# Kernel tuning notes

Measured on AMD Instinct MI355X. Metric: run time of the kernel, lower is better.

The kernel has to match this reference:

```python
import jax, jax.numpy as jnp
import numpy as np


def setup_inputs() -> dict:
    key = jax.random.key(0)
    k0, k1, k2, k3 = jax.random.split(key, 4)
    T, B, K, L, DEG = 2000, 2048, 64, 64, 3
    return {
        "currents": jax.random.normal(k0, (T, B), dtype=jnp.float32),
        "a": jax.random.normal(k1, (K,), dtype=jnp.float32) * 0.05,
        "b_lag": jax.random.normal(k2, (L,), dtype=jnp.float32) * 1e-3,
        "poly_coeff": jax.random.normal(k3, (1, DEG + 1), dtype=jnp.float32) * 0.3,
        "b_act": jnp.zeros((1,), dtype=jnp.float32),
        "max_current": jnp.full((1,), 100.0, dtype=jnp.float32),
        "max_firing_rate": jnp.full((1,), 100.0, dtype=jnp.float32),
    }


def _poly_act(z, poly_coeff, b_act, max_current, max_firing_rate):
    # PolynomialActivation.forward: x=(z-b)/max_current; poly=sum_d x^d * coeff_d^2
    x = (z - b_act[0]) / max_current[0]  # [B]
    deg = poly_coeff.shape[1] - 1
    coeff = (poly_coeff ** 2)[0]  # [deg+1]
    # build integer powers safely (negative bases) via repeated multiply
    pows = [jnp.ones_like(x)]
    for _ in range(deg):
        pows.append(pows[-1] * x)
    powers = jnp.stack(pows, axis=-1)  # [B, deg+1]
    poly = powers @ coeff  # [B]
    return jax.nn.relu(max_firing_rate[0] * jnp.tanh(poly))


def reference(currents, a, b_lag, poly_coeff, b_act, max_current, max_firing_rate):
    T, B = currents.shape
    K, L = a.shape[0], b_lag.shape[0]

    def step(carry, c_t):
        cur_buf, fs_buf = carry  # [B,K], [B,L]
        cur_buf = jnp.concatenate([cur_buf[:, 1:], c_t[:, None]], axis=1)
        x = cur_buf @ a                      # einsum('j,ij->i')
        y = 1000.0 * (fs_buf @ b_lag)        # einsum('j,ij->i')
        f = _poly_act(x + y, poly_coeff, b_act, max_current, max_firing_rate)
        fs_buf = jnp.concatenate([fs_buf[:, 1:], f[:, None]], axis=1)
        return (cur_buf, fs_buf), f

    init = (jnp.zeros((B, K), currents.dtype), jnp.zeros((B, L), currents.dtype))
    _, fs = jax.lax.scan(step, init, currents)  # fs: [T, B]
    return fs
```

## Files before the change

kernel.cpp:

```cpp
#include <hip/hip_runtime.h>

#define T_STEPS 2000
#define BATCH   2048

__global__ __launch_bounds__(256) void fused_kernel(
    const float* __restrict__ currents, const float* __restrict__ a,
    const float* __restrict__ b_lag, const float* __restrict__ poly_coeff,
    const float* __restrict__ b_act, const float* __restrict__ max_current,
    const float* __restrict__ max_firing_rate, float* __restrict__ out)
{
    int tid  = threadIdx.x;
    int lane = tid & 63;
    int wid  = tid >> 6;
    int b    = blockIdx.x * 4 + wid;

    float inv = 1.0f / max_current[0];
    float cba = -b_act[0] * inv;
    float af  = a[63 - lane] * inv;
    float gam = (1000.0f * inv) * b_lag[63 - lane];

    const float K2 = 2.8853900817779268f;
    float c0 = poly_coeff[0], c1 = poly_coeff[1], c2 = poly_coeff[2], c3 = poly_coeff[3];
    float k0 = K2 * c0 * c0, k1 = K2 * c1 * c1, k2 = K2 * c2 * c2, k3 = K2 * c3 * c3;
    float M  = max_firing_rate[0];
    float m2 = -2.0f * M;

    auto bcast = [](float v, int l) {
        return __builtin_bit_cast(float,
            __builtin_amdgcn_readlane(__builtin_bit_cast(int, v), l));
    };
    auto rotl1 = [](float v) {
        int i = __builtin_bit_cast(int, v);
        return __builtin_bit_cast(float,
            __builtin_amdgcn_update_dpp(i, i, 0x134, 0xf, 0xf, false));
    };

    const float* ccol   = currents + b;
    float*       outcol = out + b;

    float R  = cba;
    float cv = ccol[(long)lane * BATCH];
    float fv = 0.0f;

    auto step = [&](int s) {
        float c = bcast(cv, s);
        R = fmaf(af, c, R);
        float u = bcast(R, 0);
        float u2 = u * u;
        float a1 = fmaf(u, k1, k0);
        float a2 = fmaf(u, k3, k2);
        float p  = fmaf(u2, a2, a1);
        float e  = __builtin_amdgcn_exp2f(p);
        float r  = __builtin_amdgcn_rcpf(e + 1.0f);
        float f  = fmaxf(fmaf(m2, r, M), 0.0f);
        float Rr = rotl1(R);
        Rr = (lane == 63) ? cba : Rr;
        R  = fmaf(gam, f, Rr);
        fv = (lane == s) ? f : fv;
    };

    for (int chunk = 0; chunk < 31; ++chunk) {
        int t0 = chunk * 64;
        int tp = t0 + 64 + lane;
        float cv_next = (tp < T_STEPS) ? ccol[(long)tp * BATCH] : 0.0f;
#pragma unroll
        for (int s = 0; s < 64; ++s) step(s);
        outcol[(long)(t0 + lane) * BATCH] = fv;
        cv = cv_next;
    }
#pragma unroll
    for (int s = 0; s < 16; ++s) step(s);
    if (lane < 16) outcol[(long)(1984 + lane) * BATCH] = fv;
}

extern "C" void kernel_launch(void* const* d_in, const int* in_sizes, int n_in,
                              void* d_out, int out_size, void* d_ws, size_t ws_size,
                              hipStream_t stream) {
    const float* currents   = (const float*)d_in[0];
    const float* a          = (const float*)d_in[1];
    const float* b_lag      = (const float*)d_in[2];
    const float* poly_coeff = (const float*)d_in[3];
    const float* b_act      = (const float*)d_in[4];
    const float* mc         = (const float*)d_in[5];
    const float* mfr        = (const float*)d_in[6];
    float* out = (float*)d_out;

    fused_kernel<<<BATCH / 4, 256, 0, stream>>>(
        currents, a, b_lag, poly_coeff, b_act, mc, mfr, out);
}
```

Baseline: 211.3 us.

## Split into parallel convolution kernel and packed 16-column recurrence kernel

Moves the feed-forward FIR over currents out of the serial loop into a separate, fully parallel convolution kernel that writes pre-activations into the output buffer. The recurrence kernel then packs 16 batch columns per wave, four lanes per column each holding 16 lag taps in a register ring, and uses quad DPP broadcasts instead of readlane. The aim is to shorten the per-step serial dependency chain and use more lanes per wave. In exchange it adds an extra pass over memory, a large unrolled register footprint, and only 128 single-wave blocks for the recurrence.

New measurement: 253.6 us. 1.2x slower.

```diff
diff --git a/kernel.cpp b/kernel.cpp
--- a/kernel.cpp
+++ b/kernel.cpp
@@ -2,75 +2,132 @@
 
 #define T_STEPS 2000
 #define BATCH   2048
+#define TT      16
+#define NCHUNK  125
 
-__global__ __launch_bounds__(256) void fused_kernel(
+template<int CTRL>
+__device__ __forceinline__ float dppf(float v) {
+    int i = __builtin_bit_cast(int, v);
+    return __builtin_bit_cast(float,
+        __builtin_amdgcn_update_dpp(i, i, CTRL, 0xf, 0xf, true));
+}
+
+__global__ __launch_bounds__(64) void conv_kernel(
     const float* __restrict__ currents, const float* __restrict__ a,
-    const float* __restrict__ b_lag, const float* __restrict__ poly_coeff,
     const float* __restrict__ b_act, const float* __restrict__ max_current,
-    const float* __restrict__ max_firing_rate, float* __restrict__ out)
+    float* __restrict__ X)
 {
-    int tid  = threadIdx.x;
-    int lane = tid & 63;
-    int wid  = tid >> 6;
-    int b    = blockIdx.x * 4 + wid;
+    int lane = threadIdx.x;
+    int t0   = blockIdx.x * TT;
+    int c    = blockIdx.y * 64 + lane;
 
     float inv = 1.0f / max_current[0];
-    float cba = -b_act[0] * inv;
-    float af  = a[63 - lane] * inv;
-    float gam = (1000.0f * inv) * b_lag[63 - lane];
+    float cb  = -b_act[0] * inv;
+
+    float cur[TT + 63];
+#pragma unroll
+    for (int rr = 0; rr < TT + 63; ++rr) {
+        int r = t0 - 63 + rr;
+        cur[rr] = (r >= 0) ? currents[(long)r * BATCH + c] : 0.0f;
+    }
+#pragma unroll
+    for (int i = 0; i < TT; ++i) {
+        float acc = 0.0f;
+#pragma unroll
+        for (int k = 0; k < 64; ++k)
+            acc = fmaf(a[k], cur[i + k], acc);
+        X[(long)(t0 + i) * BATCH + c] = fmaf(acc, inv, cb);
+    }
+}
+
+__global__ __launch_bounds__(64) void rec_kernel(
+    const float* X,
+    const float* __restrict__ b_lag, const float* __restrict__ poly_coeff,
+    const float* __restrict__ max_current, const float* __restrict__ max_firing_rate,
+    float* out)
+{
+    int lane = threadIdx.x;
+    int q    = lane & 3;
+    int cc   = lane >> 2;
+    long col = (long)blockIdx.x * 16 + cc;
+
+    float inv    = 1.0f / max_current[0];
+    float gscale = 1000.0f * inv;
+    float tap[16];
+#pragma unroll
+    for (int j = 0; j < 16; ++j)
+        tap[j] = gscale * b_lag[63 - (16 * q + j)];
 
     const float K2 = 2.8853900817779268f;
     float c0 = poly_coeff[0], c1 = poly_coeff[1], c2 = poly_coeff[2], c3 = poly_coeff[3];
-    float k0 = K2 * c0 * c0, k1 = K2 * c1 * c1, k2 = K2 * c2 * c2, k3 = K2 * c3 * c3;
+    float k0 = K2*c0*c0, k1 = K2*c1*c1, k2 = K2*c2*c2, k3 = K2*c3*c3;
     float M  = max_firing_rate[0];
     float m2 = -2.0f * M;
 
-    auto bcast = [](float v, int l) {
-        return __builtin_bit_cast(float,
-            __builtin_amdgcn_readlane(__builtin_bit_cast(int, v), l));
-    };
-    auto rotl1 = [](float v) {
-        int i = __builtin_bit_cast(int, v);
-        return __builtin_bit_cast(float,
-            __builtin_amdgcn_update_dpp(i, i, 0x134, 0xf, 0xf, false));
-    };
+    bool e0 = (q == 0), e1 = (q == 1), e2 = (q == 2), q3 = (q == 3);
 
-    const float* ccol   = currents + b;
-    float*       outcol = out + b;
+    float ring[16];
+#pragma unroll
+    for (int j = 0; j < 16; ++j) ring[j] = 0.0f;
 
-    float R  = cba;
-    float cv = ccol[(long)lane * BATCH];
-    float fv = 0.0f;
+    const float* xp = X + col;
+    float*       op = out + col;
 
-    auto step = [&](int s) {
-        float c = bcast(cv, s);
-        R = fmaf(af, c, R);
-        float u = bcast(R, 0);
-        float u2 = u * u;
-        float a1 = fmaf(u, k1, k0);
-        float a2 = fmaf(u, k3, k2);
-        float p  = fmaf(u2, a2, a1);
-        float e  = __builtin_amdgcn_exp2f(p);
-        float r  = __builtin_amdgcn_rcpf(e + 1.0f);
-        float f  = fmaxf(fmaf(m2, r, M), 0.0f);
-        float Rr = rotl1(R);
-        Rr = (lane == 63) ? cba : Rr;
-        R  = fmaf(gam, f, Rr);
-        fv = (lane == s) ? f : fv;
-    };
+    float xa0 = xp[(long)(0  + q) * BATCH];
+    float xa1 = xp[(long)(4  + q) * BATCH];
+    float xa2 = xp[(long)(8  + q) * BATCH];
+    float xa3 = xp[(long)(12 + q) * BATCH];
 
-    for (int chunk = 0; chunk < 31; ++chunk) {
-        int t0 = chunk * 64;
-        int tp = t0 + 64 + lane;
-        float cv_next = (tp < T_STEPS) ? ccol[(long)tp * BATCH] : 0.0f;
+    for (int ch = 0; ch < NCHUNK; ++ch) {
+        long tn = (long)(ch + 1) * 16;
+        float xb0 = 0.f, xb1 = 0.f, xb2 = 0.f, xb3 = 0.f;
+        if (tn < T_STEPS) {
+            xb0 = xp[(tn + 0 ) * BATCH + (long)q * BATCH];
+            xb1 = xp[(tn + 4 ) * BATCH + (long)q * BATCH];
+            xb2 = xp[(tn + 8 ) * BATCH + (long)q * BATCH];
+            xb3 = xp[(tn + 12) * BATCH + (long)q * BATCH];
+        }
+        float fv0 = 0.f, fv1 = 0.f, fv2 = 0.f, fv3 = 0.f;
 #pragma unroll
-        for (int s = 0; s < 64; ++s) step(s);
-        outcol[(long)(t0 + lane) * BATCH] = fv;
-        cv = cv_next;
+        for (int phi = 0; phi < 16; ++phi) {
+            float xsrc = (phi < 4) ? xa0 : (phi < 8) ? xa1 : (phi < 12) ? xa2 : xa3;
+            float x_bc;
+            if      ((phi & 3) == 0) x_bc = dppf<0x00>(xsrc);
+            else if ((phi & 3) == 1) x_bc = dppf<0x55>(xsrc);
+            else if ((phi & 3) == 2) x_bc = dppf<0xAA>(xsrc);
+            else                     x_bc = dppf<0xFF>(xsrc);
+
+            float u0 = ring[phi] + x_bc;
+            float u  = dppf<0x00>(u0);
+            float u2 = u * u;
+            float a1 = fmaf(u, k1, k0);
+            float a2 = fmaf(u, k3, k2);
+            float p  = fmaf(u2, a2, a1);
+            float e  = __builtin_amdgcn_exp2f(p);
+            float r_ = __builtin_amdgcn_rcpf(e + 1.0f);
+            float f  = fmaxf(fmaf(m2, r_, M), 0.0f);
+
+            bool sel = ((phi & 3) == 0) ? e0 : ((phi & 3) == 1) ? e1
+                     : ((phi & 3) == 2) ? e2 : q3;
+            if      (phi < 4)  fv0 = sel ? f : fv0;
+            else if (phi < 8)  fv1 = sel ? f : fv1;
+            else if (phi < 12) fv2 = sel ? f : fv2;
+            else               fv3 = sel ? f : fv3;
+
+            float sh = dppf<0x101>(ring[phi]);
+            ring[phi] = q3 ? 0.0f : sh;
+
+#pragma unroll
+            for (int p2 = 0; p2 < 16; ++p2)
+                ring[p2] = fmaf(tap[(p2 - 1 - phi) & 15], f, ring[p2]);
+        }
+        long t0 = (long)ch * 16;
+        op[(t0 + 0  + q) * BATCH] = fv0;
+        op[(t0 + 4  + q) * BATCH] = fv1;
+        op[(t0 + 8  + q) * BATCH] = fv2;
+        op[(t0 + 12 + q) * BATCH] = fv3;
+        xa0 = xb0; xa1 = xb1; xa2 = xb2; xa3 = xb3;
     }
-#pragma unroll
-    for (int s = 0; s < 16; ++s) step(s);
-    if (lane < 16) outcol[(long)(1984 + lane) * BATCH] = fv;
 }
 
 extern "C" void kernel_launch(void* const* d_in, const int* in_sizes, int n_in,
@@ -85,6 +142,6 @@
     const float* mfr        = (const float*)d_in[6];
     float* out = (float*)d_out;
 
-    fused_kernel<<<BATCH / 4, 256, 0, stream>>>(
-        currents, a, b_lag, poly_coeff, b_act, mc, mfr, out);
+    conv_kernel<<<dim3(NCHUNK, BATCH / 64), 64, 0, stream>>>(currents, a, b_act, mc, out);
+    rec_kernel<<<BATCH / 16, 64, 0, stream>>>(out, b_lag, poly_coeff, mc, mfr, out);
 }
```

## Split each batch column across four lanes with packed FMA lag updates and rational tanh

Applied to the files above, without the earlier changes.

Each batch column now uses four lanes instead of a full 64-lane wave, so one wave handles 16 columns. Each lane keeps a 16-entry slice of the pending lag contributions in packed float2 registers and updates it with packed FMAs, replacing the per-step readlane broadcast and single-lane critical path. tanh(exp) is replaced by a Padé-style rational approximation with a Newton-refined reciprocal. This cuts wasted lanes and serial latency but adds more register pressure, launches fewer waves (128 blocks of 64 threads), and changes the numerics of the activation.

After: 261.0 us. 23.6% more time.

```diff
diff --git a/kernel.cpp b/kernel.cpp
--- a/kernel.cpp
+++ b/kernel.cpp
@@ -3,74 +3,123 @@
 #define T_STEPS 2000
 #define BATCH   2048
 
-__global__ __launch_bounds__(256) void fused_kernel(
+typedef float v2f __attribute__((ext_vector_type(2)));
+
+template<int CTRL>
+__device__ __forceinline__ float dppf(float v) {
+    int i = __builtin_bit_cast(int, v);
+    return __builtin_bit_cast(float,
+        __builtin_amdgcn_update_dpp(i, i, CTRL, 0xf, 0xf, true));
+}
+
+__global__ __launch_bounds__(64, 1) void fused_kernel(
     const float* __restrict__ currents, const float* __restrict__ a,
     const float* __restrict__ b_lag, const float* __restrict__ poly_coeff,
     const float* __restrict__ b_act, const float* __restrict__ max_current,
     const float* __restrict__ max_firing_rate, float* __restrict__ out)
 {
-    int tid  = threadIdx.x;
-    int lane = tid & 63;
-    int wid  = tid >> 6;
-    int b    = blockIdx.x * 4 + wid;
+    int lane = threadIdx.x;
+    int q    = lane & 3;
+    long col = (long)blockIdx.x * 16 + (lane >> 2);
 
-    float inv = 1.0f / max_current[0];
-    float cba = -b_act[0] * inv;
-    float af  = a[63 - lane] * inv;
-    float gam = (1000.0f * inv) * b_lag[63 - lane];
+    float inv  = 1.0f / max_current[0];
+    float g    = 1000.0f * inv;
+    float cb   = -b_act[0] * inv;
+    float a63i = a[63] * inv;
 
-    const float K2 = 2.8853900817779268f;
+    int mb = q << 4;
+    v2f FA[8], FB[8], CA[8], CB[8];
+#pragma unroll
+    for (int j = 0; j < 8; ++j) {
+        auto tv = [&](int jl) { return g * b_lag[63 - (mb + jl)]; };
+        auto cv = [&](int jl) {
+            int d = mb + jl + 1;
+            return (d <= 63) ? inv * a[63 - d] : 0.0f;
+        };
+        FA[j] = (v2f){ tv(2*j),            tv(2*j + 1)          };
+        FB[j] = (v2f){ tv((2*j + 1) & 15), tv((2*j + 2) & 15)   };
+        CA[j] = (v2f){ cv(2*j),            cv(2*j + 1)          };
+        CB[j] = (v2f){ cv((2*j + 1) & 15), cv((2*j + 2) & 15)   };
+    }
+
     float c0 = poly_coeff[0], c1 = poly_coeff[1], c2 = poly_coeff[2], c3 = poly_coeff[3];
-    float k0 = K2 * c0 * c0, k1 = K2 * c1 * c1, k2 = K2 * c2 * c2, k3 = K2 * c3 * c3;
+    float k0 = c0*c0, k1 = c1*c1, k2 = c2*c2, k3 = c3*c3;
     float M  = max_firing_rate[0];
-    float m2 = -2.0f * M;
+    float c105M = 105.0f * M, c945M = 945.0f * M;
 
-    auto bcast = [](float v, int l) {
-        return __builtin_bit_cast(float,
-            __builtin_amdgcn_readlane(__builtin_bit_cast(int, v), l));
-    };
-    auto rotl1 = [](float v) {
-        int i = __builtin_bit_cast(int, v);
-        return __builtin_bit_cast(float,
-            __builtin_amdgcn_update_dpp(i, i, 0x134, 0xf, 0xf, false));
-    };
+    bool q3m = (q == 3);
 
-    const float* ccol   = currents + b;
-    float*       outcol = out + b;
+    v2f P[8];
+#pragma unroll
+    for (int k = 0; k < 8; ++k) P[k] = (v2f){ cb, cb };
 
-    float R  = cba;
-    float cv = ccol[(long)lane * BATCH];
-    float fv = 0.0f;
+    const float* cp = currents + col;
+    float*       op = out + col;
 
-    auto step = [&](int s) {
-        float c = bcast(cv, s);
-        R = fmaf(af, c, R);
-        float u = bcast(R, 0);
+    float xc[8], xn[8];
+#pragma unroll
+    for (int i = 0; i < 8; ++i) xc[i] = cp[(long)i * BATCH];
+
+    auto dostep = [&](int phi, float cval, int t) {
+        float uraw = P[phi >> 1][phi & 1];
+        float u  = fmaf(a63i, cval, uraw);
         float u2 = u * u;
         float a1 = fmaf(u, k1, k0);
         float a2 = fmaf(u, k3, k2);
         float p  = fmaf(u2, a2, a1);
-        float e  = __builtin_amdgcn_exp2f(p);
-        float r  = __builtin_amdgcn_rcpf(e + 1.0f);
-        float f  = fmaxf(fmaf(m2, r, M), 0.0f);
-        float Rr = rotl1(R);
-        Rr = (lane == 63) ? cba : Rr;
-        R  = fmaf(gam, f, Rr);
-        fv = (lane == s) ? f : fv;
+        float z  = p * p;
+        float z2 = z * z;
+        float dn = fmaf(z2, 15.0f, fmaf(z, 420.0f, 945.0f));
+        float nm = p * fmaf(z, fmaf(z, M, c105M), c945M);
+        float r  = __builtin_bit_cast(float, 0x7EF311C2 - __builtin_bit_cast(int, dn));
+        r = r * fmaf(-dn, r, 2.0f);
+        r = r * fmaf(-dn, r, 2.0f);
+        float f0 = __builtin_amdgcn_fmed3f(nm * r, 0.0f, M);
+        float f  = dppf<0x00>(f0);
+        op[(long)t * BATCH] = f;
+        float pulled = dppf<0xF9>(uraw);
+        P[phi >> 1][phi & 1] = q3m ? cb : pulled;
+        v2f ff  = (v2f){ f, f };
+        v2f cc2 = (v2f){ cval, cval };
+        const int kc = ((phi + 1) & 15) >> 1;
+        if (phi & 1) {
+            const int off = ((phi + 1) >> 1) & 7;
+#pragma unroll
+            for (int kk = 0; kk < 8; ++kk) {
+                int k = (kc + kk) & 7, idx = (k - off) & 7;
+                P[k] = __builtin_elementwise_fma(FA[idx], ff,  P[k]);
+                P[k] = __builtin_elementwise_fma(CA[idx], cc2, P[k]);
+            }
+        } else {
+            const int off = ((phi >> 1) + 1) & 7;
+#pragma unroll
+            for (int kk = 0; kk < 8; ++kk) {
+                int k = (kc + kk) & 7, idx = (k - off) & 7;
+                P[k] = __builtin_elementwise_fma(FB[idx], ff,  P[k]);
+                P[k] = __builtin_elementwise_fma(CB[idx], cc2, P[k]);
+            }
+        }
     };
 
-    for (int chunk = 0; chunk < 31; ++chunk) {
-        int t0 = chunk * 64;
-        int tp = t0 + 64 + lane;
-        float cv_next = (tp < T_STEPS) ? ccol[(long)tp * BATCH] : 0.0f;
+    for (int ch = 0; ch < 125; ++ch) {
+        int t0 = ch * 16;
 #pragma unroll
-        for (int s = 0; s < 64; ++s) step(s);
-        outcol[(long)(t0 + lane) * BATCH] = fv;
-        cv = cv_next;
+        for (int gph = 0; gph < 2; ++gph) {
+            int tf = t0 + (gph + 1) * 8;
+            if (tf < T_STEPS) {
+#pragma unroll
+                for (int i = 0; i < 8; ++i) xn[i] = cp[(long)(tf + i) * BATCH];
+            } else {
+#pragma unroll
+                for (int i = 0; i < 8; ++i) xn[i] = 0.0f;
+            }
+#pragma unroll
+            for (int i = 0; i < 8; ++i)
+                dostep(gph * 8 + i, xc[i], t0 + gph * 8 + i);
+#pragma unroll
+            for (int i = 0; i < 8; ++i) xc[i] = xn[i];
+        }
     }
-#pragma unroll
-    for (int s = 0; s < 16; ++s) step(s);
-    if (lane < 16) outcol[(long)(1984 + lane) * BATCH] = fv;
 }
 
 extern "C" void kernel_launch(void* const* d_in, const int* in_sizes, int n_in,
@@ -85,6 +134,6 @@
     const float* mfr        = (const float*)d_in[6];
     float* out = (float*)d_out;
 
-    fused_kernel<<<BATCH / 4, 256, 0, stream>>>(
+    fused_kernel<<<BATCH / 16, 64, 0, stream>>>(
         currents, a, b_lag, poly_coeff, b_act, mc, mfr, out);
 }
```
